# Kernel tuning notes

Hardware: AMD Instinct MI355X
Metric: run time of the kernel (lower is better)

Reference implementation:

```python
import jax, jax.numpy as jnp
import numpy as np

HEADS = 8
DIM = 512
SCALE = (DIM // HEADS) ** (-0.5)  # 0.125


def setup_inputs() -> dict:
    key = jax.random.key(0)
    k1, k2, k3, k4 = jax.random.split(key, 4)
    B, C, H, W = 4, DIM, 96, 96
    x = jax.random.normal(k1, (B, C, H, W), dtype=jnp.float32)
    # 1x1 conv weights collapsed to matrices [out_ch, in_ch]
    w_qkv = jax.random.normal(k2, (3 * DIM, DIM), dtype=jnp.float32) * (DIM ** -0.5)
    w_out = jax.random.normal(k3, (DIM, DIM), dtype=jnp.float32) * (DIM ** -0.5)
    b_out = jax.random.normal(k4, (DIM,), dtype=jnp.float32) * 0.01
    return {"x": x, "w_qkv": w_qkv, "w_out": w_out, "b_out": b_out}


def reference(x, w_qkv, w_out, b_out):
    # axis='height' branch of the original forward
    b, c, h, w = x.shape
    heads = HEADS
    d = c // heads
    # 1x1 conv == per-pixel GEMM: [B,3C,H,W]
    qkv = jnp.einsum('bchw,oc->bohw', x, w_qkv)
    # 'b (qkv heads d) x y -> qkv b heads x y d'
    qkv = qkv.reshape(b, 3, heads, d, h, w)
    qkv = jnp.transpose(qkv, (1, 0, 2, 4, 5, 3))  # [3, b, heads, h, w, d]
    q, k, v = qkv[0], qkv[1], qkv[2]
    # attention along the width axis, batched over (b, heads, row x)
    dots = jnp.einsum('bhxid,bhxjd->bhxij', q, k) * SCALE
    attn = jax.nn.softmax(dots, axis=-1)
    out = jnp.einsum('bhxij,bhxjd->bhxid', attn, v)  # [b, heads, h, w, d]
    # 'b heads x y d -> b (heads d) x y'
    out = jnp.transpose(out, (0, 1, 4, 2, 3)).reshape(b, heads * d, h, w)
    # to_out 1x1 conv with bias
    out = jnp.einsum('bchw,oc->bohw', out, w_out) + b_out[None, :, None, None]
    return out
```

## Files before the change

kernel.cpp:

```cpp
#include <hip/hip_runtime.h>

typedef unsigned short u16;
typedef unsigned int u32;
typedef __attribute__((ext_vector_type(8))) short short8;
typedef __attribute__((ext_vector_type(4))) float floatx4;

#define HEADS 8
#define DIM 512
#define HH 96
#define WW 96
#define NPIX 9216
#define M_TOT 36864
#define N_QKV 1536
#define SCALE 0.125f

__device__ __forceinline__ float b2f(u16 v){
    union{float f;u32 u;}x; x.u=((u32)v)<<16; return x.f;
}
__device__ __forceinline__ u16 f2b(float f){
    union{float f;u32 u;}x; x.f=f;
    u32 u=x.u + 0x7fffu + ((x.u>>16)&1u);
    return (u16)(u>>16);
}
__device__ __forceinline__ u32 pack2(float a,float b){
    u32 r; asm("v_cvt_pk_bf16_f32 %0, %1, %2" : "=v"(r) : "v"(a), "v"(b));
    return r;
}

__device__ __forceinline__ void gload16(const u16* g, u16* l){
    __builtin_amdgcn_global_load_lds(
        (const __attribute__((address_space(1))) u32*)g,
        (__attribute__((address_space(3))) u32*)l, 16, 0, 0);
}

__global__ void detect_dtype(const u16* __restrict__ wq, int* __restrict__ flag){
    __shared__ int cnt;
    if (threadIdx.x==0) cnt=0;
    __syncthreads();
    u16 u = wq[2*threadIdx.x];
    int e = (u>>7)&0xff;
    if (e>=100 && e<=128) atomicAdd(&cnt,1);
    __syncthreads();
    if (threadIdx.x==0) *flag = (cnt>128)?1:0;
}

__global__ __launch_bounds__(256)
void convert_w(const void* __restrict__ wq, const void* __restrict__ wo,
               const int* __restrict__ flag, u16* __restrict__ wqb, u16* __restrict__ wob){
    const int isb = *flag;
    int i = blockIdx.x*256 + threadIdx.x;
    const int nq = N_QKV*DIM;
    if (i < nq){
        wqb[i] = isb ? ((const u16*)wq)[i] : f2b(((const float*)wq)[i]);
    } else {
        int j = i - nq;
        wob[j] = isb ? ((const u16*)wo)[j] : f2b(((const float*)wo)[j]);
    }
}

__global__ __launch_bounds__(256)
void convert_x(const void* __restrict__ xv, const int* __restrict__ flag,
               u16* __restrict__ xb){
    __shared__ u16 tile[64][65];
    const int isb = *flag;
    const int p0 = blockIdx.x*64, c0 = blockIdx.y*64, b = blockIdx.z;
    const int t = threadIdx.x;
    const int pl = t&63, c4 = t>>6;
    const float* x32 = (const float*)xv;
    const u16*   x16 = (const u16*)xv;
    size_t src = ((size_t)b*DIM + c0 + c4)*NPIX + p0 + pl;
    #pragma unroll
    for (int i=0;i<16;i++){
        int cl = c4 + i*4;
        size_t s = src + (size_t)i*4*NPIX;
        tile[cl][pl] = isb ? x16[s] : f2b(x32[s]);
    }
    __syncthreads();
    const int cu = t&31, r8 = t>>5;
    u32* xb32 = (u32*)xb;
    #pragma unroll
    for (int i=0;i<8;i++){
        int pr = r8 + i*8;
        u32 v = (u32)tile[2*cu][pr] | ((u32)tile[2*cu+1][pr]<<16);
        xb32[((size_t)b*NPIX + p0 + pr)*(DIM/2) + (c0>>1) + cu] = v;
    }
}

__global__ __launch_bounds__(512, 2)
void gemm_qkv(const u16* __restrict__ A, const u16* __restrict__ B,
              u16* __restrict__ qkt, u16* __restrict__ vtt){
    __shared__ __align__(16) union ShMem {
        u16 tiles[65536];
        float ctQ[8][16][68];
        float ctV[8][16][132];
    } sh;
    u16* lds = sh.tiles;
    const int id = blockIdx.x;
    const int xcd = id & 7, slot = id >> 3;
    const int q6 = slot/6;
    const int by = xcd*18 + q6;
    const int bx = slot - q6*6;
    const int t = threadIdx.x;
    const int w = t>>6, l = t&63, lr = l&15, lq = l>>4;
    const int wm2 = w>>2, wn4 = w&3;
    const int m0 = by*256, n0 = bx*256;
    const u16* gA0 = A + (size_t)(m0 +       w*16 + lr)*DIM + lq*8;
    const u16* gA1 = A + (size_t)(m0 + 128 + w*16 + lr)*DIM + lq*8;
    const u16* gB0 = B + (size_t)(n0 +       w*16 + lr)*DIM + lq*8;
    const u16* gB1 = B + (size_t)(n0 + 128 + w*16 + lr)*DIM + lq*8;

#define STG(gp, opb, h, ko, bb) do { \
        const u16* _g = (gp) + (ko); \
        u16* _l = lds + (bb)*32768 + (opb) + ((h)*8 + w)*1024; \
        gload16(_g,      _l); \
        gload16(_g + 32, _l + 512); \
    } while(0)

    floatx4 acc[8][4] = {};
    STG(gA0, 0,     0, 0, 0);
    STG(gA1, 0,     1, 0, 0);
    STG(gB0, 16384, 0, 0, 0);
    STG(gB1, 16384, 1, 0, 0);

    #pragma unroll 1
    for (int ktile=0; ktile<8; ++ktile){
        const int cur = ktile&1, nxt = cur^1;
        const int ko = (ktile+1)*64;
        if (ktile < 7){
            STG(gA0, 0, 0, ko, nxt);
            asm volatile("s_waitcnt vmcnt(2)" ::: "memory");
        } else {
            asm volatile("s_waitcnt vmcnt(0)" ::: "memory");
        }
        __builtin_amdgcn_s_barrier();
        asm volatile("" ::: "memory");
        const u16* bA = lds + cur*32768 +         wm2*8192 + l*8;
        const u16* bB = lds + cur*32768 + 16384 + wn4*4096 + l*8;
        short8 af[4][2], blo[2][2], bhi[2][2];
        #pragma unroll
        for (int mi=0;mi<4;mi++){
            af[mi][0] = *(const short8*)(bA + mi*1024);
            af[mi][1] = *(const short8*)(bA + mi*1024 + 512);
        }
        #pragma unroll
        for (int ni=0;ni<2;ni++){
            blo[ni][0] = *(const short8*)(bB + ni*1024);
            blo[ni][1] = *(const short8*)(bB + ni*1024 + 512);
        }
        if (ktile < 7) STG(gA1, 0, 1, ko, nxt);
        asm volatile("" ::: "memory");
        __builtin_amdgcn_s_barrier();
        __builtin_amdgcn_sched_barrier(0);
        __builtin_amdgcn_s_setprio(1);
        #pragma unroll
        for (int mi=0;mi<4;mi++)
            #pragma unroll
            for (int ni=0;ni<2;ni++){
                acc[mi][ni] = __builtin_amdgcn_mfma_f32_16x16x32_bf16(af[mi][0], blo[ni][0], acc[mi][ni], 0,0,0);
                acc[mi][ni] = __builtin_amdgcn_mfma_f32_16x16x32_bf16(af[mi][1], blo[ni][1], acc[mi][ni], 0,0,0);
            }
        __builtin_amdgcn_s_setprio(0);
        __builtin_amdgcn_sched_barrier(0);
        __builtin_amdgcn_s_barrier();
        #pragma unroll
        for (int ni=0;ni<2;ni++){
            bhi[ni][0] = *(const short8*)(bB + (2+ni)*1024);
            bhi[ni][1] = *(const short8*)(bB + (2+ni)*1024 + 512);
        }
        if (ktile < 7) STG(gB0, 16384, 0, ko, nxt);
        asm volatile("" ::: "memory");
        __builtin_amdgcn_s_barrier();
        __builtin_amdgcn_sched_barrier(0);
        __builtin_amdgcn_s_setprio(1);
        #pragma unroll
        for (int mi=0;mi<4;mi++)
            #pragma unroll
            for (int ni=0;ni<2;ni++){
                acc[mi][2+ni] = __builtin_amdgcn_mfma_f32_16x16x32_bf16(af[mi][0], bhi[ni][0], acc[mi][2+ni], 0,0,0);
                acc[mi][2+ni] = __builtin_amdgcn_mfma_f32_16x16x32_bf16(af[mi][1], bhi[ni][1], acc[mi][2+ni], 0,0,0);
            }
        __builtin_amdgcn_s_setprio(0);
        __builtin_amdgcn_sched_barrier(0);
        __builtin_amdgcn_s_barrier();
        #pragma unroll
        for (int mi=0;mi<4;mi++){
            af[mi][0] = *(const short8*)(bA + (4+mi)*1024);
            af[mi][1] = *(const short8*)(bA + (4+mi)*1024 + 512);
        }
        if (ktile < 7) STG(gB1, 16384, 1, ko, nxt);
        asm volatile("" ::: "memory");
        __builtin_amdgcn_s_barrier();
        __builtin_amdgcn_sched_barrier(0);
        __builtin_amdgcn_s_setprio(1);
        #pragma unroll
        for (int mi=0;mi<4;mi++)
            #pragma unroll
            for (int ni=0;ni<2;ni++){
                acc[4+mi][2+ni] = __builtin_amdgcn_mfma_f32_16x16x32_bf16(af[mi][0], bhi[ni][0], acc[4+mi][2+ni], 0,0,0);
                acc[4+mi][2+ni] = __builtin_amdgcn_mfma_f32_16x16x32_bf16(af[mi][1], bhi[ni][1], acc[4+mi][2+ni], 0,0,0);
            }
        __builtin_amdgcn_s_setprio(0);
        __builtin_amdgcn_sched_barrier(0);
        __builtin_amdgcn_s_barrier();
        __builtin_amdgcn_s_setprio(1);
        #pragma unroll
        for (int mi=0;mi<4;mi++)
            #pragma unroll
            for (int ni=0;ni<2;ni++){
                acc[4+mi][ni] = __builtin_amdgcn_mfma_f32_16x16x32_bf16(af[mi][0], blo[ni][0], acc[4+mi][ni], 0,0,0);
                acc[4+mi][ni] = __builtin_amdgcn_mfma_f32_16x16x32_bf16(af[mi][1], blo[ni][1], acc[4+mi][ni], 0,0,0);
            }
        __builtin_amdgcn_s_setprio(0);
        __builtin_amdgcn_sched_barrier(0);
        asm volatile("" ::: "memory");
        __builtin_amdgcn_s_barrier();
        asm volatile("" ::: "memory");
    }
#undef STG
    const int bat   = m0 / NPIX;
    const int p0img = (m0 - bat*NPIX) + wm2*128;
    if (bx < 4){
        float (*ct)[68] = sh.ctQ[w];
        const int nbase = n0 + wn4*64;
        const int isK   = (nbase >= 512);
        const int head  = (nbase - (isK ? 512 : 0)) >> 6;
        const int kqoff = isK ? 6144 : 0;
        const size_t blk0 = (size_t)(bat*8 + head)*96;
        #pragma unroll
        for (int mi=0;mi<8;mi++){
            #pragma unroll
            for (int ni=0;ni<4;ni++)
                #pragma unroll
                for (int r=0;r<4;r++)
                    ct[lq*4+r][ni*16+lr] = acc[mi][ni][r];
            int pv  = (p0img + mi*16) >> 4;
            int row = pv/6, mt = pv - row*6;
            u16* dst = qkt + (blk0 + row)*12288 + kqoff + mt*1024 + l*8;
            #pragma unroll
            for (int ks=0;ks<2;ks++){
                const float* cp = &ct[l&15][ks*32 + (l>>4)*8];
                float4 v0 = *(const float4*)(cp);
                float4 v1 = *(const float4*)(cp+4);
                uint4 s;
                s.x=pack2(v0.x,v0.y); s.y=pack2(v0.z,v0.w);
                s.z=pack2(v1.x,v1.y); s.w=pack2(v1.z,v1.w);
                *((uint4*)(dst + ks*512)) = s;
            }
        }
    } else {
        float (*ct)[132] = sh.ctV[w];
        const int head = ((n0 - 1024) + wn4*64) >> 6;
        const size_t blk0 = (size_t)(bat*8 + head)*96;
        for (int ni=0; ni<4; ni++){
            #pragma unroll
            for (int mi=0;mi<8;mi++)
                #pragma unroll
                for (int r=0;r<4;r++)
                    ct[lr][mi*16 + lq*4 + r] = acc[mi][ni][r];
            #pragma unroll
            for (int cc=0;cc<4;cc++){
                int p32 = (p0img + cc*32) >> 5;
                int row = p32/3, jt = p32 - row*3;
                const float* cp = &ct[l&15][cc*32 + (l>>4)*8];
                float4 v0 = *(const float4*)(cp);
                float4 v1 = *(const float4*)(cp+4);
                uint4 s;
                s.x=pack2(v0.x,v0.y); s.y=pack2(v0.z,v0.w);
                s.z=pack2(v1.x,v1.y); s.w=pack2(v1.z,v1.w);
                *((uint4*)(vtt + (blk0 + row)*6144 + (ni*3 + jt)*512 + l*8)) = s;
            }
        }
    }
}

__global__ __launch_bounds__(256)
void attn_kernel(const u16* __restrict__ qkt, const u16* __restrict__ vtt,
                 u16* __restrict__ attno){
    __shared__ __align__(16) u16 Qf[6144];
    __shared__ __align__(16) u16 Pb[9984];
    __shared__ float Ss[96][97];
    __shared__ float smax[96][2], ssum[96][2], rinv[96];
    const int t = threadIdx.x;
    const int w = t>>6, l = t&63, lr = l&15, lq = l>>4;
    const int wm = w&1, wn = w>>1;
    const int blk = blockIdx.x;
    const int row  = blk % HH;
    const int bh   = blk / HH;
    const int head = bh & 7;
    const int bat  = bh >> 3;
    const size_t pixrow = (size_t)bat*NPIX + row*WW;
    const u16* qkbase = qkt + (size_t)blk*12288;
    #pragma unroll
    for (int i=0;i<6;i++){
        int c  = w*6 + i;
        u16* dst = ((c<12) ? Qf + c*512 : Pb + (c-12)*512) + l*8;
        gload16(qkbase + c*512 + l*8, dst);
    }
    __syncthreads();
    {
        floatx4 acc[3][3] = {};
        #pragma unroll
        for (int ks=0;ks<2;ks++){
            short8 af[3], bf[3];
            #pragma unroll
            for (int i=0;i<3;i++) af[i] = *(const short8*)&Qf[((wm*3+i)*2+ks)*512 + l*8];
            #pragma unroll
            for (int j=0;j<3;j++) bf[j] = *(const short8*)&Pb[((wn*3+j)*2+ks)*512 + l*8];
            #pragma unroll
            for (int i=0;i<3;i++)
                #pragma unroll
                for (int j=0;j<3;j++)
                    acc[i][j] = __builtin_amdgcn_mfma_f32_16x16x32_bf16(af[i], bf[j], acc[i][j], 0,0,0);
        }
        #pragma unroll
        for (int i=0;i<3;i++)
            #pragma unroll
            for (int j=0;j<3;j++)
                #pragma unroll
                for (int r=0;r<4;r++)
                    Ss[(wm*3+i)*16 + lq*4 + r][(wn*3+j)*16 + lr] = acc[i][j][r]*SCALE;
    }
    __syncthreads();
    {
        const u16* vbase = vtt + (size_t)blk*6144;
        #pragma unroll
        for (int i=0;i<3;i++){
            int c = w*3 + i;
            gload16(vbase + c*512 + l*8, Qf + c*512 + l*8);
        }
    }
    const int srow = t>>1, shalf = t&1, sbase = shalf*48;
    if (t < 192){
        float m = -1e30f;
        #pragma unroll 8
        for (int j=0;j<48;j++) m = fmaxf(m, Ss[srow][sbase+j]);
        smax[srow][shalf] = m;
    }
    __syncthreads();
    if (t < 192){
        float m2 = fmaxf(smax[srow][0], smax[srow][1]);
        float s = 0.f;
        u32* prow = (u32*)&Pb[srow*104 + sbase];
        #pragma unroll 8
        for (int j=0;j<48;j+=2){
            float e0 = __expf(Ss[srow][sbase+j]   - m2);
            float e1 = __expf(Ss[srow][sbase+j+1] - m2);
            prow[j>>1] = pack2(e0, e1);
            s += e0 + e1;
        }
        ssum[srow][shalf] = s;
    }
    __syncthreads();
    if (t < 192 && shalf==0) rinv[srow] = 1.f/(ssum[srow][0]+ssum[srow][1]);
    floatx4 o[3][2] = {};
    #pragma unroll
    for (int ks2=0;ks2<3;ks2++){
        short8 bf2[2];
        #pragma unroll
        for (int bb=0;bb<2;bb++)
            bf2[bb] = *(const short8*)&Qf[((wn*2+bb)*3+ks2)*512 + l*8];
        #pragma unroll
        for (int aa=0;aa<3;aa++){
            short8 af = *(const short8*)&Pb[((wm*3+aa)*16+lr)*104 + ks2*32 + lq*8];
            #pragma unroll
            for (int bb=0;bb<2;bb++)
                o[aa][bb] = __builtin_amdgcn_mfma_f32_16x16x32_bf16(af, bf2[bb], o[aa][bb], 0,0,0);
        }
    }
    __syncthreads();
    #pragma unroll
    for (int aa=0;aa<3;aa++){
        #pragma unroll
        for (int r=0;r<4;r++){
            int m = (wm*3+aa)*16 + lq*4 + r;
            float rv = rinv[m];
            int d0 = wn*32 + lr;
            Pb[m*72 + d0]      = f2b(o[aa][0][r]*rv);
            Pb[m*72 + d0 + 16] = f2b(o[aa][1][r]*rv);
        }
    }
    __syncthreads();
    #pragma unroll
    for (int i=0;i<3;i++){
        int idx = i*256 + t;
        int rr = idx>>3, seg = idx&7;
        uint4 vv = *(const uint4*)&Pb[rr*72 + seg*8];
        *(uint4*)(attno + (pixrow+rr)*512 + head*64 + seg*8) = vv;
    }
}

__global__ __launch_bounds__(512, 2)
void gemm_out(const u16* __restrict__ A, const u16* __restrict__ B,
              const void* __restrict__ bias, const int* __restrict__ flag,
              void* __restrict__ outv){
    __shared__ __align__(16) union ShMem {
        u16 tiles[49152];
        float ct[8][16][68];
    } sh;
    u16* lds = sh.tiles;
    const int id = blockIdx.x;
    const int xcd = id & 7, slot = id >> 3;
    const int by = xcd*18 + (slot>>2);
    const int bx = slot & 3;
    const int t = threadIdx.x;
    const int w = t>>6, l = t&63, lr = l&15, lq = l>>4;
    const int wm4 = w>>1, wn2 = w&1;
    const int m0 = by*256, n0 = bx*128;
    const u16* gA = A + (size_t)(m0 + w*16 + lr)*DIM + lq*8;
    const u16* gB = B + (size_t)(n0 + w*16 + lr)*DIM + lq*8;

#define STG_A(h, ko, bb) do { \
        const u16* _g = gA + (size_t)(h)*65536 + (ko); \
        u16* _l = lds + (bb)*24576 + ((h)*8 + w)*1024; \
        gload16(_g,      _l); \
        gload16(_g + 32, _l + 512); \
    } while(0)
#define STG_B(ko, bb) do { \
        const u16* _g = gB + (ko); \
        u16* _l = lds + (bb)*24576 + 16384 + w*1024; \
        gload16(_g,      _l); \
        gload16(_g + 32, _l + 512); \
    } while(0)

    floatx4 acc[4][4] = {};
    STG_A(0,0,0); STG_A(1,0,0); STG_B(0,0);

    #pragma unroll 1
    for (int kt=0; kt<8; ++kt){
        const int cur = kt&1, nxt = cur^1;
        const int ko = (kt+1)*64;
        if (kt < 7){
            STG_A(0, ko, nxt);
            asm volatile("s_waitcnt vmcnt(2)" ::: "memory");
        } else {
            asm volatile("s_waitcnt vmcnt(0)" ::: "memory");
        }
        __builtin_amdgcn_s_barrier();
        asm volatile("" ::: "memory");
        const u16* bA = lds + cur*24576 +         wm4*4096 + l*8;
        const u16* bB = lds + cur*24576 + 16384 + wn2*4096 + l*8;
        short8 af[4][2], bf[2][2];
        #pragma unroll
        for (int mi=0;mi<4;mi++){
            af[mi][0] = *(const short8*)(bA + mi*1024);
            af[mi][1] = *(const short8*)(bA + mi*1024 + 512);
        }
        #pragma unroll
        for (int ni=0;ni<2;ni++){
            bf[ni][0] = *(const short8*)(bB + ni*1024);
            bf[ni][1] = *(const short8*)(bB + ni*1024 + 512);
        }
        if (kt < 7) STG_A(1, ko, nxt);
        asm volatile("" ::: "memory");
        __builtin_amdgcn_s_barrier();
        __builtin_amdgcn_sched_barrier(0);
        __builtin_amdgcn_s_setprio(1);
        #pragma unroll
        for (int mi=0;mi<4;mi++)
            #pragma unroll
            for (int ni=0;ni<2;ni++){
                acc[mi][ni] = __builtin_amdgcn_mfma_f32_16x16x32_bf16(af[mi][0], bf[ni][0], acc[mi][ni], 0,0,0);
                acc[mi][ni] = __builtin_amdgcn_mfma_f32_16x16x32_bf16(af[mi][1], bf[ni][1], acc[mi][ni], 0,0,0);
            }
        __builtin_amdgcn_s_setprio(0);
        __builtin_amdgcn_sched_barrier(0);
        __builtin_amdgcn_s_barrier();
        #pragma unroll
        for (int ni=0;ni<2;ni++){
            bf[ni][0] = *(const short8*)(bB + (2+ni)*1024);
            bf[ni][1] = *(const short8*)(bB + (2+ni)*1024 + 512);
        }
        if (kt < 7) STG_B(ko, nxt);
        asm volatile("" ::: "memory");
        __builtin_amdgcn_s_barrier();
        __builtin_amdgcn_sched_barrier(0);
        __builtin_amdgcn_s_setprio(1);
        #pragma unroll
        for (int mi=0;mi<4;mi++)
            #pragma unroll
            for (int ni=0;ni<2;ni++){
                acc[mi][2+ni] = __builtin_amdgcn_mfma_f32_16x16x32_bf16(af[mi][0], bf[ni][0], acc[mi][2+ni], 0,0,0);
                acc[mi][2+ni] = __builtin_amdgcn_mfma_f32_16x16x32_bf16(af[mi][1], bf[ni][1], acc[mi][2+ni], 0,0,0);
            }
        __builtin_amdgcn_s_setprio(0);
        __builtin_amdgcn_sched_barrier(0);
        asm volatile("" ::: "memory");
        __builtin_amdgcn_s_barrier();
        asm volatile("" ::: "memory");
    }
#undef STG_A
#undef STG_B
    const int isb = *flag;
    const int bat  = m0 / NPIX;
    const int pix0 = (m0 - bat*NPIX) + wm4*64;
    float (*ct)[68] = sh.ct[w];
    const u16*   b16 = (const u16*)bias;
    const float* b32 = (const float*)bias;
    const int nl = l>>2, seg = l&3;
    for (int ni=0; ni<4; ni++){
        #pragma unroll
        for (int mi=0;mi<4;mi++)
            #pragma unroll
            for (int r=0;r<4;r++)
                ct[lr][mi*16 + lq*4 + r] = acc[mi][ni][r];
        int ng = n0 + wn2*64 + ni*16 + nl;
        float bv = isb ? b2f(b16[ng]) : b32[ng];
        const float* cp = &ct[nl][seg*16];
        float4 v0 = *(const float4*)(cp);
        float4 v1 = *(const float4*)(cp+4);
        float4 v2 = *(const float4*)(cp+8);
        float4 v3 = *(const float4*)(cp+12);
        v0.x+=bv; v0.y+=bv; v0.z+=bv; v0.w+=bv;
        v1.x+=bv; v1.y+=bv; v1.z+=bv; v1.w+=bv;
        v2.x+=bv; v2.y+=bv; v2.z+=bv; v2.w+=bv;
        v3.x+=bv; v3.y+=bv; v3.z+=bv; v3.w+=bv;
        size_t off = ((size_t)(bat*DIM + ng))*NPIX + pix0 + seg*16;
        if (isb){
            uint4 s0, s1;
            s0.x=pack2(v0.x,v0.y); s0.y=pack2(v0.z,v0.w);
            s0.z=pack2(v1.x,v1.y); s0.w=pack2(v1.z,v1.w);
            s1.x=pack2(v2.x,v2.y); s1.y=pack2(v2.z,v2.w);
            s1.z=pack2(v3.x,v3.y); s1.w=pack2(v3.z,v3.w);
            *(uint4*)((u16*)outv + off)     = s0;
            *(uint4*)((u16*)outv + off + 8) = s1;
        } else {
            float* of = (float*)outv + off;
            *(float4*)(of)    = v0;
            *(float4*)(of+4)  = v1;
            *(float4*)(of+8)  = v2;
            *(float4*)(of+12) = v3;
        }
    }
}

extern "C" void kernel_launch(void* const* d_in, const int* in_sizes, int n_in,
                              void* d_out, int out_size, void* d_ws, size_t ws_size,
                              hipStream_t stream){
    const void* x    = d_in[0];
    const void* wqkv = d_in[1];
    const void* wout = d_in[2];
    const void* bout = d_in[3];
    char* wsb = (char*)d_ws;
    int* flag    = (int*)wsb;
    u16* xb      = (u16*)(wsb + 256);
    u16* attn_ws = xb;
    u16* wqb     = xb + (size_t)M_TOT*DIM;
    u16* wob     = wqb + (size_t)N_QKV*DIM;
    u16* qk_ws   = wob + (size_t)DIM*DIM;
    u16* vt_ws   = qk_ws + (size_t)M_TOT*1024;
    detect_dtype<<<1, 256, 0, stream>>>((const u16*)wqkv, flag);
    convert_w<<<4096, 256, 0, stream>>>(wqkv, wout, flag, wqb, wob);
    convert_x<<<dim3(144, 8, 4), 256, 0, stream>>>(x, flag, xb);
    gemm_qkv<<<864, 512, 0, stream>>>(xb, wqb, qk_ws, vt_ws);
    attn_kernel<<<3072, 256, 0, stream>>>(qk_ws, vt_ws, attn_ws);
    gemm_out<<<576, 512, 0, stream>>>(attn_ws, wob, bout, flag, d_out);
}
```

Before: 340.3 us.

## Register-resident per-wave attention and smaller 128x128 tiles for output GEMM

```diff
diff --git a/kernel.cpp b/kernel.cpp
--- a/kernel.cpp
+++ b/kernel.cpp
@@ -25,6 +25,9 @@
 __device__ __forceinline__ u32 pack2(float a,float b){
     u32 r; asm("v_cvt_pk_bf16_f32 %0, %1, %2" : "=v"(r) : "v"(a), "v"(b));
     return r;
+}
+__device__ __forceinline__ short8 mk8(u32 a,u32 b,u32 c,u32 d){
+    union{u32 u[4]; short8 v;} x; x.u[0]=a; x.u[1]=b; x.u[2]=c; x.u[3]=d; return x.v;
 }
 
 __device__ __forceinline__ void gload16(const u16* g, u16* l){
@@ -276,154 +279,117 @@
 __global__ __launch_bounds__(256)
 void attn_kernel(const u16* __restrict__ qkt, const u16* __restrict__ vtt,
                  u16* __restrict__ attno){
-    __shared__ __align__(16) u16 Qf[6144];
-    __shared__ __align__(16) u16 Pb[9984];
-    __shared__ float Ss[96][97];
-    __shared__ float smax[96][2], ssum[96][2], rinv[96];
     const int t = threadIdx.x;
     const int w = t>>6, l = t&63, lr = l&15, lq = l>>4;
-    const int wm = w&1, wn = w>>1;
-    const int blk = blockIdx.x;
-    const int row  = blk % HH;
-    const int bh   = blk / HH;
-    const int head = bh & 7;
-    const int bat  = bh >> 3;
-    const size_t pixrow = (size_t)bat*NPIX + row*WW;
-    const u16* qkbase = qkt + (size_t)blk*12288;
-    #pragma unroll
-    for (int i=0;i<6;i++){
-        int c  = w*6 + i;
-        u16* dst = ((c<12) ? Qf + c*512 : Pb + (c-12)*512) + l*8;
-        gload16(qkbase + c*512 + l*8, dst);
-    }
-    __syncthreads();
-    {
-        floatx4 acc[3][3] = {};
-        #pragma unroll
-        for (int ks=0;ks<2;ks++){
-            short8 af[3], bf[3];
-            #pragma unroll
-            for (int i=0;i<3;i++) af[i] = *(const short8*)&Qf[((wm*3+i)*2+ks)*512 + l*8];
-            #pragma unroll
-            for (int j=0;j<3;j++) bf[j] = *(const short8*)&Pb[((wn*3+j)*2+ks)*512 + l*8];
-            #pragma unroll
-            for (int i=0;i<3;i++)
-                #pragma unroll
-                for (int j=0;j<3;j++)
-                    acc[i][j] = __builtin_amdgcn_mfma_f32_16x16x32_bf16(af[i], bf[j], acc[i][j], 0,0,0);
-        }
-        #pragma unroll
-        for (int i=0;i<3;i++)
-            #pragma unroll
-            for (int j=0;j<3;j++)
-                #pragma unroll
-                for (int r=0;r<4;r++)
-                    Ss[(wm*3+i)*16 + lq*4 + r][(wn*3+j)*16 + lr] = acc[i][j][r]*SCALE;
-    }
-    __syncthreads();
-    {
-        const u16* vbase = vtt + (size_t)blk*6144;
-        #pragma unroll
-        for (int i=0;i<3;i++){
-            int c = w*3 + i;
-            gload16(vbase + c*512 + l*8, Qf + c*512 + l*8);
-        }
-    }
-    const int srow = t>>1, shalf = t&1, sbase = shalf*48;
-    if (t < 192){
-        float m = -1e30f;
-        #pragma unroll 8
-        for (int j=0;j<48;j++) m = fmaxf(m, Ss[srow][sbase+j]);
-        smax[srow][shalf] = m;
-    }
-    __syncthreads();
-    if (t < 192){
-        float m2 = fmaxf(smax[srow][0], smax[srow][1]);
-        float s = 0.f;
-        u32* prow = (u32*)&Pb[srow*104 + sbase];
-        #pragma unroll 8
-        for (int j=0;j<48;j+=2){
-            float e0 = __expf(Ss[srow][sbase+j]   - m2);
-            float e1 = __expf(Ss[srow][sbase+j+1] - m2);
-            prow[j>>1] = pack2(e0, e1);
-            s += e0 + e1;
-        }
-        ssum[srow][shalf] = s;
-    }
-    __syncthreads();
-    if (t < 192 && shalf==0) rinv[srow] = 1.f/(ssum[srow][0]+ssum[srow][1]);
-    floatx4 o[3][2] = {};
-    #pragma unroll
-    for (int ks2=0;ks2<3;ks2++){
-        short8 bf2[2];
-        #pragma unroll
-        for (int bb=0;bb<2;bb++)
-            bf2[bb] = *(const short8*)&Qf[((wn*2+bb)*3+ks2)*512 + l*8];
-        #pragma unroll
-        for (int aa=0;aa<3;aa++){
-            short8 af = *(const short8*)&Pb[((wm*3+aa)*16+lr)*104 + ks2*32 + lq*8];
-            #pragma unroll
-            for (int bb=0;bb<2;bb++)
-                o[aa][bb] = __builtin_amdgcn_mfma_f32_16x16x32_bf16(af, bf2[bb], o[aa][bb], 0,0,0);
-        }
-    }
-    __syncthreads();
-    #pragma unroll
-    for (int aa=0;aa<3;aa++){
-        #pragma unroll
-        for (int r=0;r<4;r++){
-            int m = (wm*3+aa)*16 + lq*4 + r;
-            float rv = rinv[m];
-            int d0 = wn*32 + lr;
-            Pb[m*72 + d0]      = f2b(o[aa][0][r]*rv);
-            Pb[m*72 + d0 + 16] = f2b(o[aa][1][r]*rv);
-        }
-    }
-    __syncthreads();
-    #pragma unroll
-    for (int i=0;i<3;i++){
-        int idx = i*256 + t;
-        int rr = idx>>3, seg = idx&7;
-        uint4 vv = *(const uint4*)&Pb[rr*72 + seg*8];
-        *(uint4*)(attno + (pixrow+rr)*512 + head*64 + seg*8) = vv;
-    }
-}
-
-__global__ __launch_bounds__(512, 2)
+    const int id  = blockIdx.x;
+    const int bid = (id&7)*576 + (id>>3);
+    const int widx = bid*4 + w;
+    const int qt   = widx % 6;
+    const int rowu = widx / 6;
+    const int row  = rowu % HH;
+    const int bh   = rowu / HH;
+    const int head = bh & 7, bat = bh >> 3;
+    const u16* qkb = qkt + (size_t)rowu*12288;
+    const u16* vb  = vtt + (size_t)rowu*6144;
+    short8 qf0 = *(const short8*)(qkb + (qt*2+0)*512 + l*8);
+    short8 qf1 = *(const short8*)(qkb + (qt*2+1)*512 + l*8);
+    floatx4 s[6];
+    #pragma unroll
+    for (int jt=0;jt<6;jt++){
+        short8 k0 = *(const short8*)(qkb + 6144 + (jt*2+0)*512 + l*8);
+        short8 k1 = *(const short8*)(qkb + 6144 + (jt*2+1)*512 + l*8);
+        floatx4 a = {};
+        a = __builtin_amdgcn_mfma_f32_16x16x32_bf16(k0, qf0, a, 0,0,0);
+        a = __builtin_amdgcn_mfma_f32_16x16x32_bf16(k1, qf1, a, 0,0,0);
+        s[jt] = a;
+    }
+    float m = -1e30f;
+    #pragma unroll
+    for (int jt=0;jt<6;jt++)
+        #pragma unroll
+        for (int r=0;r<4;r++){ s[jt][r] *= SCALE; m = fmaxf(m, s[jt][r]); }
+    m = fmaxf(m, __shfl_xor(m, 16));
+    m = fmaxf(m, __shfl_xor(m, 32));
+    float sum = 0.f;
+    u32 pk0[6], pk1[6];
+    #pragma unroll
+    for (int jt=0;jt<6;jt++){
+        float e0 = __expf(s[jt][0]-m), e1 = __expf(s[jt][1]-m);
+        float e2 = __expf(s[jt][2]-m), e3 = __expf(s[jt][3]-m);
+        sum += e0+e1+e2+e3;
+        pk0[jt] = pack2(e0,e1);
+        pk1[jt] = pack2(e2,e3);
+    }
+    sum += __shfl_xor(sum, 16);
+    sum += __shfl_xor(sum, 32);
+    const float rinv = 1.f/sum;
+    const int srcA = lr + ((lq&1)<<5);
+    const int srcB = srcA + 16;
+    const int hi   = lq>>1;
+    short8 pf[3];
+    #pragma unroll
+    for (int kb=0;kb<3;kb++){
+        u32 x0=__shfl(pk0[kb*2],srcA), y0=__shfl(pk0[kb*2+1],srcA);
+        u32 x1=__shfl(pk1[kb*2],srcA), y1=__shfl(pk1[kb*2+1],srcA);
+        u32 x2=__shfl(pk0[kb*2],srcB), y2=__shfl(pk0[kb*2+1],srcB);
+        u32 x3=__shfl(pk1[kb*2],srcB), y3=__shfl(pk1[kb*2+1],srcB);
+        pf[kb] = mk8(hi?y0:x0, hi?y1:x1, hi?y2:x2, hi?y3:x3);
+    }
+    floatx4 o[4] = {};
+    #pragma unroll
+    for (int kb=0;kb<3;kb++){
+        #pragma unroll
+        for (int dt=0;dt<4;dt++){
+            short8 vf = *(const short8*)(vb + (dt*3+kb)*512 + l*8);
+            o[dt] = __builtin_amdgcn_mfma_f32_16x16x32_bf16(vf, pf[kb], o[dt], 0,0,0);
+        }
+    }
+    const size_t pixrow = (size_t)bat*NPIX + row*WW + qt*16;
+    u16* ob = attno + (pixrow + lr)*512 + head*64 + lq*4;
+    #pragma unroll
+    for (int dt=0;dt<4;dt++){
+        uint2 st;
+        st.x = pack2(o[dt][0]*rinv, o[dt][1]*rinv);
+        st.y = pack2(o[dt][2]*rinv, o[dt][3]*rinv);
+        *(uint2*)(ob + dt*16) = st;
+    }
+}
+
+__global__ __launch_bounds__(256, 2)
 void gemm_out(const u16* __restrict__ A, const u16* __restrict__ B,
               const void* __restrict__ bias, const int* __restrict__ flag,
               void* __restrict__ outv){
     __shared__ __align__(16) union ShMem {
-        u16 tiles[49152];
-        float ct[8][16][68];
+        u16 tiles[32768];
+        float ct[4][16][68];
     } sh;
     u16* lds = sh.tiles;
     const int id = blockIdx.x;
     const int xcd = id & 7, slot = id >> 3;
-    const int by = xcd*18 + (slot>>2);
+    const int by = xcd*36 + (slot>>2);
     const int bx = slot & 3;
     const int t = threadIdx.x;
     const int w = t>>6, l = t&63, lr = l&15, lq = l>>4;
-    const int wm4 = w>>1, wn2 = w&1;
-    const int m0 = by*256, n0 = bx*128;
+    const int wm = w>>1, wn = w&1;
+    const int m0 = by*128, n0 = bx*128;
     const u16* gA = A + (size_t)(m0 + w*16 + lr)*DIM + lq*8;
     const u16* gB = B + (size_t)(n0 + w*16 + lr)*DIM + lq*8;
 
 #define STG_A(h, ko, bb) do { \
-        const u16* _g = gA + (size_t)(h)*65536 + (ko); \
-        u16* _l = lds + (bb)*24576 + ((h)*8 + w)*1024; \
+        const u16* _g = gA + (size_t)(h)*32768 + (ko); \
+        u16* _l = lds + (bb)*16384 + ((h)*4 + w)*1024; \
         gload16(_g,      _l); \
         gload16(_g + 32, _l + 512); \
     } while(0)
-#define STG_B(ko, bb) do { \
-        const u16* _g = gB + (ko); \
-        u16* _l = lds + (bb)*24576 + 16384 + w*1024; \
+#define STG_B(h, ko, bb) do { \
+        const u16* _g = gB + (size_t)(h)*32768 + (ko); \
+        u16* _l = lds + (bb)*16384 + 8192 + ((h)*4 + w)*1024; \
         gload16(_g,      _l); \
         gload16(_g + 32, _l + 512); \
     } while(0)
 
     floatx4 acc[4][4] = {};
-    STG_A(0,0,0); STG_A(1,0,0); STG_B(0,0);
+    STG_A(0,0,0); STG_A(1,0,0); STG_B(0,0,0); STG_B(1,0,0);
 
     #pragma unroll 1
     for (int kt=0; kt<8; ++kt){
@@ -437,8 +403,8 @@
         }
         __builtin_amdgcn_s_barrier();
         asm volatile("" ::: "memory");
-        const u16* bA = lds + cur*24576 +         wm4*4096 + l*8;
-        const u16* bB = lds + cur*24576 + 16384 + wn2*4096 + l*8;
+        const u16* bA = lds + cur*16384 +        wm*4096 + l*8;
+        const u16* bB = lds + cur*16384 + 8192 + wn*4096 + l*8;
         short8 af[4][2], bf[2][2];
         #pragma unroll
         for (int mi=0;mi<4;mi++){
@@ -470,7 +436,7 @@
             bf[ni][0] = *(const short8*)(bB + (2+ni)*1024);
             bf[ni][1] = *(const short8*)(bB + (2+ni)*1024 + 512);
         }
-        if (kt < 7) STG_B(ko, nxt);
+        if (kt < 7){ STG_B(0, ko, nxt); STG_B(1, ko, nxt); }
         asm volatile("" ::: "memory");
         __builtin_amdgcn_s_barrier();
         __builtin_amdgcn_sched_barrier(0);
@@ -492,7 +458,7 @@
 #undef STG_B
     const int isb = *flag;
     const int bat  = m0 / NPIX;
-    const int pix0 = (m0 - bat*NPIX) + wm4*64;
+    const int pix0 = (m0 - bat*NPIX) + wm*64;
     float (*ct)[68] = sh.ct[w];
     const u16*   b16 = (const u16*)bias;
     const float* b32 = (const float*)bias;
@@ -503,7 +469,7 @@
             #pragma unroll
             for (int r=0;r<4;r++)
                 ct[lr][mi*16 + lq*4 + r] = acc[mi][ni][r];
-        int ng = n0 + wn2*64 + ni*16 + nl;
+        int ng = n0 + wn*64 + ni*16 + nl;
         float bv = isb ? b2f(b16[ng]) : b32[ng];
         const float* cp = &ct[nl][seg*16];
         float4 v0 = *(const float4*)(cp);
@@ -552,6 +518,6 @@
     convert_w<<<4096, 256, 0, stream>>>(wqkv, wout, flag, wqb, wob);
     convert_x<<<dim3(144, 8, 4), 256, 0, stream>>>(x, flag, xb);
     gemm_qkv<<<864, 512, 0, stream>>>(xb, wqb, qk_ws, vt_ws);
-    attn_kernel<<<3072, 256, 0, stream>>>(qk_ws, vt_ws, attn_ws);
-    gemm_out<<<576, 512, 0, stream>>>(attn_ws, wob, bout, flag, d_out);
-}
+    attn_kernel<<<4608, 256, 0, stream>>>(qk_ws, vt_ws, attn_ws);
+    gemm_out<<<1152, 256, 0, stream>>>(attn_ws, wob, bout, flag, d_out);
+}
```

New measurement: 323.8 us. -4.9%, faster.
